# Kernel optimization log

Hardware: AMD Instinct MI355X
Metric: run time of the kernel (lower is better)

## Reference

```python
import jax, jax.numpy as jnp
import numpy as np

B, T, F_IN = 8, 32768, 64
N, F, HID = 64, 64, 32


def setup_inputs() -> dict:
    key = jax.random.key(0)
    ks = jax.random.split(key, 10)
    x = jax.random.normal(ks[0], (B, T, F_IN), dtype=jnp.float32)
    # pre_mlp: Dense(32) -> relu -> Dense(F)
    W1 = jax.random.normal(ks[1], (F_IN, HID), dtype=jnp.float32) * (1.0 / np.sqrt(F_IN))
    b1 = jnp.zeros((HID,), dtype=jnp.float32)
    W2 = jax.random.normal(ks[2], (HID, F), dtype=jnp.float32) * (1.0 / np.sqrt(HID))
    b2 = jnp.zeros((F,), dtype=jnp.float32)
    # SSM params (inits mirror the flax module)
    Lambda_raw = -0.7 * jnp.ones((N,), dtype=jnp.float32)
    P = jax.random.normal(ks[3], (N,), dtype=jnp.float32) * 0.02
    Wu = jax.random.normal(ks[4], (F,), dtype=jnp.float32) * 0.02
    C = jax.random.normal(ks[5], (N,), dtype=jnp.float32) * 0.02
    D = jax.random.normal(ks[6], (F,), dtype=jnp.float32) * 0.02
    b_y = jnp.zeros((), dtype=jnp.float32)
    return {"x": x, "W1": W1, "b1": b1, "W2": W2, "b2": b2,
            "Lambda_raw": Lambda_raw, "P": P, "Wu": Wu, "C": C, "D": D, "b_y": b_y}


def reference(x, W1, b1, W2, b2, Lambda_raw, P, Wu, C, D, b_y):
    # pre_mlp: per-timestep feature projection
    h = jax.nn.relu(jnp.einsum('bti,ih->bth', x, W1) + b1)
    feats = jnp.einsum('bth,hf->btf', h, W2) + b2          # (B,T,F)
    # scalar drive per timestep
    u = jnp.einsum('btf,f->bt', feats, Wu)                 # (B,T)
    # stable diagonal decay in (0,1): Lambda = -softplus(raw), A = exp(Lambda)
    A = jnp.exp(-jax.nn.softplus(Lambda_raw))              # (N,)
    Bu = u[..., None] * P                                  # (B,T,N) per-step injection

    def step(s, bu_t):                                     # s: (B,N), bu_t: (B,N)
        s = A * s + bu_t
        return s, s

    s0 = jnp.zeros((x.shape[0], Lambda_raw.shape[0]), dtype=x.dtype)
    _, states = jax.lax.scan(step, s0, jnp.swapaxes(Bu, 0, 1))  # (T,B,N)
    states = jnp.swapaxes(states, 0, 1)                    # (B,T,N)
    # readout: C-state + D-feedthrough + bias
    y = jnp.einsum('btn,n->bt', states, C) + jnp.einsum('btf,f->bt', feats, D) + b_y
    return y
```

## Files before the change

kernel.cpp:

```cpp
#include <hip/hip_runtime.h>

#define BB   8
#define TT   32768
#define FIN  64
#define HIDN 32
#define NST  64
#define FFD  64
#define WWIN 256
#define TILE 1024


typedef __attribute__((ext_vector_type(8))) short short8;
typedef __attribute__((ext_vector_type(4))) float f32x4;

static __device__ __forceinline__ unsigned short f2bf(float f) {
    unsigned int u = __builtin_bit_cast(unsigned int, f);
    unsigned int lsb = (u >> 16) & 1u;
    u += 0x7fffu + lsb;
    return (unsigned short)(u >> 16);
}

__global__ __launch_bounds__(256) void setup_kernel(
    const float* __restrict__ W1, const float* __restrict__ W2,
    const float* __restrict__ b2, const float* __restrict__ Lraw,
    const float* __restrict__ P, const float* __restrict__ Wu,
    const float* __restrict__ C, const float* __restrict__ Dv,
    const float* __restrict__ b_y, float* __restrict__ ws)
{
    int tid = threadIdx.x;
    if (tid < HIDN) {
        float su = 0.f, sd = 0.f;
        for (int f = 0; f < FFD; ++f) {
            float w2 = W2[tid * FFD + f];
            su += w2 * Wu[f];
            sd += w2 * Dv[f];
        }
        ws[tid]      = su;
        ws[32 + tid] = sd;
    }
    if (tid == 64) {
        float cu = 0.f, cd = 0.f;
        for (int f = 0; f < FFD; ++f) { cu += b2[f] * Wu[f]; cd += b2[f] * Dv[f]; }
        ws[64] = cu;
        ws[65] = cd + b_y[0];
    }
    if (tid < WWIN) {
        float acc = 0.f;
        float jf = (float)tid;
        for (int n = 0; n < NST; ++n) {
            float raw = Lraw[n];
            float sp  = fmaxf(raw, 0.f) + log1pf(expf(-fabsf(raw)));
            acc += C[n] * P[n] * __expf(-sp * jf);
        }
        ws[128 + tid] = acc;
    }
    {
        int f    = tid >> 6;
        int lane = tid & 63;
        int khalf = f & 1, ntile = f >> 1;
        int quad = lane >> 4;
        int nn   = (lane & 15) + ntile * 16;
        unsigned short h8[8];
#pragma unroll
        for (int j = 0; j < 8; ++j) {
            int k = khalf * 32 + quad * 8 + j;
            h8[j] = f2bf(W1[k * HIDN + nn]);
        }
        unsigned int w0 = (unsigned int)h8[0] | ((unsigned int)h8[1] << 16);
        unsigned int w1 = (unsigned int)h8[2] | ((unsigned int)h8[3] << 16);
        unsigned int w2 = (unsigned int)h8[4] | ((unsigned int)h8[5] << 16);
        unsigned int w3 = (unsigned int)h8[6] | ((unsigned int)h8[7] << 16);
        ((uint4*)(ws + 512))[tid] = make_uint4(w0, w1, w2, w3);
    }
}

__global__ __launch_bounds__(256) void mlp_kernel(
    const float* __restrict__ x, const float* __restrict__ b1,
    const float* __restrict__ ws, float* __restrict__ u,
    float* __restrict__ yd)
{
    int lane = threadIdx.x & 63;
    int wid  = threadIdx.x >> 6;
    int tile = blockIdx.x * 4 + wid;
    int t0   = tile * 16;
    int m    = lane & 15;
    int quad = lane >> 4;

    const short8* frp = (const short8*)(ws + 512);
    short8 bk0n0 = frp[0 * 64 + lane];
    short8 bk1n0 = frp[1 * 64 + lane];
    short8 bk0n1 = frp[2 * 64 + lane];
    short8 bk1n1 = frp[3 * 64 + lane];

    const float* xr = x + (size_t)(t0 + m) * FIN + quad * 8;
    float4 xa0 = *(const float4*)(xr);
    float4 xa1 = *(const float4*)(xr + 4);
    float4 xb0 = *(const float4*)(xr + 32);
    float4 xb1 = *(const float4*)(xr + 36);

    short8 a0, a1;
    a0[0] = (short)f2bf(xa0.x); a0[1] = (short)f2bf(xa0.y);
    a0[2] = (short)f2bf(xa0.z); a0[3] = (short)f2bf(xa0.w);
    a0[4] = (short)f2bf(xa1.x); a0[5] = (short)f2bf(xa1.y);
    a0[6] = (short)f2bf(xa1.z); a0[7] = (short)f2bf(xa1.w);
    a1[0] = (short)f2bf(xb0.x); a1[1] = (short)f2bf(xb0.y);
    a1[2] = (short)f2bf(xb0.z); a1[3] = (short)f2bf(xb0.w);
    a1[4] = (short)f2bf(xb1.x); a1[5] = (short)f2bf(xb1.y);
    a1[6] = (short)f2bf(xb1.z); a1[7] = (short)f2bf(xb1.w);

    f32x4 acc0 = {0.f, 0.f, 0.f, 0.f};
    f32x4 acc1 = {0.f, 0.f, 0.f, 0.f};
    acc0 = __builtin_amdgcn_mfma_f32_16x16x32_bf16(a0, bk0n0, acc0, 0, 0, 0);
    acc0 = __builtin_amdgcn_mfma_f32_16x16x32_bf16(a1, bk1n0, acc0, 0, 0, 0);
    acc1 = __builtin_amdgcn_mfma_f32_16x16x32_bf16(a0, bk0n1, acc1, 0, 0, 0);
    acc1 = __builtin_amdgcn_mfma_f32_16x16x32_bf16(a1, bk1n1, acc1, 0, 0, 0);

    float b1n0 = b1[m];
    float b1n1 = b1[16 + m];
    float wu0  = ws[m],      wu1 = ws[16 + m];
    float wd0  = ws[32 + m], wd1 = ws[48 + m];
    float cu   = ws[64],     cd  = ws[65];

    float ut[4], yt[4];
#pragma unroll
    for (int r = 0; r < 4; ++r) {
        float h0 = fmaxf(acc0[r] + b1n0, 0.f);
        float h1 = fmaxf(acc1[r] + b1n1, 0.f);
        ut[r] = h0 * wu0 + h1 * wu1;
        yt[r] = h0 * wd0 + h1 * wd1;
    }
#pragma unroll
    for (int mask = 1; mask <= 8; mask <<= 1) {
#pragma unroll
        for (int r = 0; r < 4; ++r) {
            ut[r] += __shfl_xor(ut[r], mask);
            yt[r] += __shfl_xor(yt[r], mask);
        }
    }
    if (m == 0) {
        int row = t0 + quad * 4;
        *(float4*)&u[row]  = make_float4(ut[0] + cu, ut[1] + cu, ut[2] + cu, ut[3] + cu);
        *(float4*)&yd[row] = make_float4(yt[0] + cd, yt[1] + cd, yt[2] + cd, yt[3] + cd);
    }
}

__global__ __launch_bounds__(256) void conv_kernel(
    const float* __restrict__ u, const float* __restrict__ K,
    float* __restrict__ y)
{
    __shared__ __align__(16) float us[WWIN + TILE];
    __shared__ __align__(16) float Ks[WWIN];

    int tid = threadIdx.x;
    const int blocksPerSeq = TT / TILE;
    int b  = blockIdx.x / blocksPerSeq;
    int t0 = (blockIdx.x % blocksPerSeq) * TILE;
    const float* ub = u + (size_t)b * TT;

    for (int s = tid; s < WWIN + TILE; s += 256) {
        int gt = t0 - WWIN + s;
        us[s] = (gt >= 0) ? ub[gt] : 0.f;
    }
    if (tid < WWIN) Ks[tid] = K[tid];
    __syncthreads();

    int base = WWIN + tid * 4;
    size_t oidx = (size_t)b * TT + t0 + tid * 4;
    float4 yv = *(const float4*)&y[oidx];
    float a0 = yv.x, a1 = yv.y, a2 = yv.z, a3 = yv.w;

#pragma unroll 8
    for (int j = 0; j < WWIN; j += 4) {
        float4 kk = *(const float4*)&Ks[j];
        float4 ua = *(const float4*)&us[base - j - 4];
        float4 ux = *(const float4*)&us[base - j];
        a0 += kk.x * ux.x + kk.y * ua.w + kk.z * ua.z + kk.w * ua.y;
        a1 += kk.x * ux.y + kk.y * ux.x + kk.z * ua.w + kk.w * ua.z;
        a2 += kk.x * ux.z + kk.y * ux.y + kk.z * ux.x + kk.w * ua.w;
        a3 += kk.x * ux.w + kk.y * ux.z + kk.z * ux.y + kk.w * ux.x;
    }
    *(float4*)&y[oidx] = make_float4(a0, a1, a2, a3);
}

extern "C" void kernel_launch(void* const* d_in, const int* in_sizes, int n_in,
                              void* d_out, int out_size, void* d_ws, size_t ws_size,
                              hipStream_t stream)
{
    const float* x    = (const float*)d_in[0];
    const float* W1   = (const float*)d_in[1];
    const float* b1   = (const float*)d_in[2];
    const float* W2   = (const float*)d_in[3];
    const float* b2   = (const float*)d_in[4];
    const float* Lraw = (const float*)d_in[5];
    const float* P    = (const float*)d_in[6];
    const float* Wu   = (const float*)d_in[7];
    const float* C    = (const float*)d_in[8];
    const float* Dv   = (const float*)d_in[9];
    const float* b_y  = (const float*)d_in[10];

    float* ws = (float*)d_ws;
    float* u  = ws + 2048;
    float* y  = (float*)d_out;

    setup_kernel<<<1, 256, 0, stream>>>(W1, W2, b2, Lraw, P, Wu, C, Dv, b_y, ws);
    mlp_kernel<<<(BB * TT / 16) / 4, 256, 0, stream>>>(x, b1, ws, u, y);
    conv_kernel<<<(BB * TT) / TILE, 256, 0, stream>>>(u, ws + 128, y);
}
```

Baseline: 140.7 us.

## Fold setup kernel into MLP and conv kernels, process four tiles per wave

```diff
diff --git a/kernel.cpp b/kernel.cpp
--- a/kernel.cpp
+++ b/kernel.cpp
@@ -8,7 +8,7 @@
 #define FFD  64
 #define WWIN 256
 #define TILE 1024
-
+#define TPW  4
 
 typedef __attribute__((ext_vector_type(8))) short short8;
 typedef __attribute__((ext_vector_type(4))) float f32x4;
@@ -20,136 +20,172 @@
     return (unsigned short)(u >> 16);
 }
 
-__global__ __launch_bounds__(256) void setup_kernel(
-    const float* __restrict__ W1, const float* __restrict__ W2,
-    const float* __restrict__ b2, const float* __restrict__ Lraw,
-    const float* __restrict__ P, const float* __restrict__ Wu,
-    const float* __restrict__ C, const float* __restrict__ Dv,
-    const float* __restrict__ b_y, float* __restrict__ ws)
+static __device__ __forceinline__ float dot8(float4 a0, float4 a1, float4 b0, float4 b1) {
+    return a0.x*b0.x + a0.y*b0.y + a0.z*b0.z + a0.w*b0.w
+         + a1.x*b1.x + a1.y*b1.y + a1.z*b1.z + a1.w*b1.w;
+}
+
+__global__ __launch_bounds__(256) void mlp_kernel(
+    const float* __restrict__ x, const float* __restrict__ W1,
+    const float* __restrict__ b1, const float* __restrict__ W2,
+    const float* __restrict__ b2, const float* __restrict__ Wu,
+    const float* __restrict__ Dv, const float* __restrict__ b_y,
+    float* __restrict__ u, float* __restrict__ yd)
 {
+    __shared__ __align__(16) uint4 fragLDS[4 * 64];
+    __shared__ float pu[32 * 8], pd[32 * 8], pc[16];
+    __shared__ float wuF[32], wdF[32], cucd[2];
+
     int tid = threadIdx.x;
-    if (tid < HIDN) {
-        float su = 0.f, sd = 0.f;
-        for (int f = 0; f < FFD; ++f) {
-            float w2 = W2[tid * FFD + f];
-            su += w2 * Wu[f];
-            sd += w2 * Dv[f];
-        }
-        ws[tid]      = su;
-        ws[32 + tid] = sd;
-    }
-    if (tid == 64) {
-        float cu = 0.f, cd = 0.f;
-        for (int f = 0; f < FFD; ++f) { cu += b2[f] * Wu[f]; cd += b2[f] * Dv[f]; }
-        ws[64] = cu;
-        ws[65] = cd + b_y[0];
-    }
-    if (tid < WWIN) {
-        float acc = 0.f;
-        float jf = (float)tid;
-        for (int n = 0; n < NST; ++n) {
-            float raw = Lraw[n];
-            float sp  = fmaxf(raw, 0.f) + log1pf(expf(-fabsf(raw)));
-            acc += C[n] * P[n] * __expf(-sp * jf);
-        }
-        ws[128 + tid] = acc;
-    }
+
     {
         int f    = tid >> 6;
         int lane = tid & 63;
         int khalf = f & 1, ntile = f >> 1;
-        int quad = lane >> 4;
-        int nn   = (lane & 15) + ntile * 16;
+        int quad  = lane >> 4;
+        int nn    = (lane & 15) + ntile * 16;
         unsigned short h8[8];
 #pragma unroll
         for (int j = 0; j < 8; ++j) {
             int k = khalf * 32 + quad * 8 + j;
             h8[j] = f2bf(W1[k * HIDN + nn]);
         }
-        unsigned int w0 = (unsigned int)h8[0] | ((unsigned int)h8[1] << 16);
-        unsigned int w1 = (unsigned int)h8[2] | ((unsigned int)h8[3] << 16);
-        unsigned int w2 = (unsigned int)h8[4] | ((unsigned int)h8[5] << 16);
-        unsigned int w3 = (unsigned int)h8[6] | ((unsigned int)h8[7] << 16);
-        ((uint4*)(ws + 512))[tid] = make_uint4(w0, w1, w2, w3);
-    }
-}
-
-__global__ __launch_bounds__(256) void mlp_kernel(
-    const float* __restrict__ x, const float* __restrict__ b1,
-    const float* __restrict__ ws, float* __restrict__ u,
-    float* __restrict__ yd)
-{
-    int lane = threadIdx.x & 63;
-    int wid  = threadIdx.x >> 6;
-    int tile = blockIdx.x * 4 + wid;
-    int t0   = tile * 16;
-    int m    = lane & 15;
-    int quad = lane >> 4;
-
-    const short8* frp = (const short8*)(ws + 512);
-    short8 bk0n0 = frp[0 * 64 + lane];
-    short8 bk1n0 = frp[1 * 64 + lane];
-    short8 bk0n1 = frp[2 * 64 + lane];
-    short8 bk1n1 = frp[3 * 64 + lane];
-
-    const float* xr = x + (size_t)(t0 + m) * FIN + quad * 8;
-    float4 xa0 = *(const float4*)(xr);
-    float4 xa1 = *(const float4*)(xr + 4);
-    float4 xb0 = *(const float4*)(xr + 32);
-    float4 xb1 = *(const float4*)(xr + 36);
-
-    short8 a0, a1;
-    a0[0] = (short)f2bf(xa0.x); a0[1] = (short)f2bf(xa0.y);
-    a0[2] = (short)f2bf(xa0.z); a0[3] = (short)f2bf(xa0.w);
-    a0[4] = (short)f2bf(xa1.x); a0[5] = (short)f2bf(xa1.y);
-    a0[6] = (short)f2bf(xa1.z); a0[7] = (short)f2bf(xa1.w);
-    a1[0] = (short)f2bf(xb0.x); a1[1] = (short)f2bf(xb0.y);
-    a1[2] = (short)f2bf(xb0.z); a1[3] = (short)f2bf(xb0.w);
-    a1[4] = (short)f2bf(xb1.x); a1[5] = (short)f2bf(xb1.y);
-    a1[6] = (short)f2bf(xb1.z); a1[7] = (short)f2bf(xb1.w);
-
-    f32x4 acc0 = {0.f, 0.f, 0.f, 0.f};
-    f32x4 acc1 = {0.f, 0.f, 0.f, 0.f};
-    acc0 = __builtin_amdgcn_mfma_f32_16x16x32_bf16(a0, bk0n0, acc0, 0, 0, 0);
-    acc0 = __builtin_amdgcn_mfma_f32_16x16x32_bf16(a1, bk1n0, acc0, 0, 0, 0);
-    acc1 = __builtin_amdgcn_mfma_f32_16x16x32_bf16(a0, bk0n1, acc1, 0, 0, 0);
-    acc1 = __builtin_amdgcn_mfma_f32_16x16x32_bf16(a1, bk1n1, acc1, 0, 0, 0);
-
-    float b1n0 = b1[m];
-    float b1n1 = b1[16 + m];
-    float wu0  = ws[m],      wu1 = ws[16 + m];
-    float wd0  = ws[32 + m], wd1 = ws[48 + m];
-    float cu   = ws[64],     cd  = ws[65];
-
-    float ut[4], yt[4];
-#pragma unroll
-    for (int r = 0; r < 4; ++r) {
-        float h0 = fmaxf(acc0[r] + b1n0, 0.f);
-        float h1 = fmaxf(acc1[r] + b1n1, 0.f);
-        ut[r] = h0 * wu0 + h1 * wu1;
-        yt[r] = h0 * wd0 + h1 * wd1;
-    }
-#pragma unroll
-    for (int mask = 1; mask <= 8; mask <<= 1) {
+        fragLDS[tid] = make_uint4(
+            (unsigned int)h8[0] | ((unsigned int)h8[1] << 16),
+            (unsigned int)h8[2] | ((unsigned int)h8[3] << 16),
+            (unsigned int)h8[4] | ((unsigned int)h8[5] << 16),
+            (unsigned int)h8[6] | ((unsigned int)h8[7] << 16));
+    }
+    {
+        int h = tid >> 3, part = tid & 7;
+        const float4* w2p = (const float4*)(W2 + h * FFD + part * 8);
+        float4 wa = w2p[0], wb = w2p[1];
+        float4 ua = *(const float4*)(Wu + part * 8);
+        float4 ub = *(const float4*)(Wu + part * 8 + 4);
+        float4 da = *(const float4*)(Dv + part * 8);
+        float4 db = *(const float4*)(Dv + part * 8 + 4);
+        pu[tid] = dot8(wa, wb, ua, ub);
+        pd[tid] = dot8(wa, wb, da, db);
+        if (tid < 8) {
+            float4 ba = *(const float4*)(b2 + tid * 8);
+            float4 bb = *(const float4*)(b2 + tid * 8 + 4);
+            float4 u2a = *(const float4*)(Wu + tid * 8);
+            float4 u2b = *(const float4*)(Wu + tid * 8 + 4);
+            pc[tid] = dot8(ba, bb, u2a, u2b);
+        } else if (tid < 16) {
+            int p = tid - 8;
+            float4 ba = *(const float4*)(b2 + p * 8);
+            float4 bb = *(const float4*)(b2 + p * 8 + 4);
+            float4 d2a = *(const float4*)(Dv + p * 8);
+            float4 d2b = *(const float4*)(Dv + p * 8 + 4);
+            pc[tid] = dot8(ba, bb, d2a, d2b);
+        }
+    }
+    __syncthreads();
+    if (tid < 32) {
+        float s = 0.f;
+#pragma unroll
+        for (int p = 0; p < 8; ++p) s += pu[tid * 8 + p];
+        wuF[tid] = s;
+    } else if (tid < 64) {
+        int h = tid - 32;
+        float s = 0.f;
+#pragma unroll
+        for (int p = 0; p < 8; ++p) s += pd[h * 8 + p];
+        wdF[h] = s;
+    } else if (tid == 64) {
+        float s = 0.f;
+#pragma unroll
+        for (int p = 0; p < 8; ++p) s += pc[p];
+        cucd[0] = s;
+    } else if (tid == 65) {
+        float s = 0.f;
+#pragma unroll
+        for (int p = 8; p < 16; ++p) s += pc[p];
+        cucd[1] = s + b_y[0];
+    }
+    __syncthreads();
+
+    int lane = tid & 63, wid = tid >> 6;
+    int m = lane & 15, quad = lane >> 4;
+
+    short8 bk0n0 = __builtin_bit_cast(short8, fragLDS[0 * 64 + lane]);
+    short8 bk1n0 = __builtin_bit_cast(short8, fragLDS[1 * 64 + lane]);
+    short8 bk0n1 = __builtin_bit_cast(short8, fragLDS[2 * 64 + lane]);
+    short8 bk1n1 = __builtin_bit_cast(short8, fragLDS[3 * 64 + lane]);
+
+    float b1n0 = b1[m],       b1n1 = b1[16 + m];
+    float wu0  = wuF[m],      wu1  = wuF[16 + m];
+    float wd0  = wdF[m],      wd1  = wdF[16 + m];
+    float cu   = cucd[0],     cd   = cucd[1];
+
+    int tbase = blockIdx.x * 256 + wid * 64;
+    const float* xr = x + (size_t)(tbase + m) * FIN + quad * 8;
+
+    float4 xv[2][4];
+#define LOADT(buf, tt) { const float* p_ = xr + (tt) * 16 * FIN;          \
+        (buf)[0] = *(const float4*)(p_);      (buf)[1] = *(const float4*)(p_ + 4);  \
+        (buf)[2] = *(const float4*)(p_ + 32); (buf)[3] = *(const float4*)(p_ + 36); }
+
+    LOADT(xv[0], 0);
+    LOADT(xv[1], 1);
+
+#pragma unroll
+    for (int tt = 0; tt < TPW; ++tt) {
+        float4 x0 = xv[tt & 1][0], x1 = xv[tt & 1][1];
+        float4 x2 = xv[tt & 1][2], x3 = xv[tt & 1][3];
+        if (tt + 2 < TPW) LOADT(xv[tt & 1], tt + 2);
+
+        short8 a0, a1;
+        a0[0] = (short)f2bf(x0.x); a0[1] = (short)f2bf(x0.y);
+        a0[2] = (short)f2bf(x0.z); a0[3] = (short)f2bf(x0.w);
+        a0[4] = (short)f2bf(x1.x); a0[5] = (short)f2bf(x1.y);
+        a0[6] = (short)f2bf(x1.z); a0[7] = (short)f2bf(x1.w);
+        a1[0] = (short)f2bf(x2.x); a1[1] = (short)f2bf(x2.y);
+        a1[2] = (short)f2bf(x2.z); a1[3] = (short)f2bf(x2.w);
+        a1[4] = (short)f2bf(x3.x); a1[5] = (short)f2bf(x3.y);
+        a1[6] = (short)f2bf(x3.z); a1[7] = (short)f2bf(x3.w);
+
+        f32x4 acc0 = {0.f, 0.f, 0.f, 0.f};
+        f32x4 acc1 = {0.f, 0.f, 0.f, 0.f};
+        acc0 = __builtin_amdgcn_mfma_f32_16x16x32_bf16(a0, bk0n0, acc0, 0, 0, 0);
+        acc0 = __builtin_amdgcn_mfma_f32_16x16x32_bf16(a1, bk1n0, acc0, 0, 0, 0);
+        acc1 = __builtin_amdgcn_mfma_f32_16x16x32_bf16(a0, bk0n1, acc1, 0, 0, 0);
+        acc1 = __builtin_amdgcn_mfma_f32_16x16x32_bf16(a1, bk1n1, acc1, 0, 0, 0);
+
+        float ut[4], yt[4];
 #pragma unroll
         for (int r = 0; r < 4; ++r) {
-            ut[r] += __shfl_xor(ut[r], mask);
-            yt[r] += __shfl_xor(yt[r], mask);
-        }
-    }
-    if (m == 0) {
-        int row = t0 + quad * 4;
-        *(float4*)&u[row]  = make_float4(ut[0] + cu, ut[1] + cu, ut[2] + cu, ut[3] + cu);
-        *(float4*)&yd[row] = make_float4(yt[0] + cd, yt[1] + cd, yt[2] + cd, yt[3] + cd);
-    }
+            float h0 = fmaxf(acc0[r] + b1n0, 0.f);
+            float h1 = fmaxf(acc1[r] + b1n1, 0.f);
+            ut[r] = h0 * wu0 + h1 * wu1;
+            yt[r] = h0 * wd0 + h1 * wd1;
+        }
+#pragma unroll
+        for (int mask = 1; mask <= 8; mask <<= 1) {
+#pragma unroll
+            for (int r = 0; r < 4; ++r) {
+                ut[r] += __shfl_xor(ut[r], mask);
+                yt[r] += __shfl_xor(yt[r], mask);
+            }
+        }
+        if (m == 0) {
+            int row = tbase + tt * 16 + quad * 4;
+            *(float4*)&u[row]  = make_float4(ut[0] + cu, ut[1] + cu, ut[2] + cu, ut[3] + cu);
+            *(float4*)&yd[row] = make_float4(yt[0] + cd, yt[1] + cd, yt[2] + cd, yt[3] + cd);
+        }
+    }
+#undef LOADT
 }
 
 __global__ __launch_bounds__(256) void conv_kernel(
-    const float* __restrict__ u, const float* __restrict__ K,
+    const float* __restrict__ u, const float* __restrict__ Lraw,
+    const float* __restrict__ P, const float* __restrict__ C,
     float* __restrict__ y)
 {
     __shared__ __align__(16) float us[WWIN + TILE];
     __shared__ __align__(16) float Ks[WWIN];
+    __shared__ float spv[NST], cpv[NST];
 
     int tid = threadIdx.x;
     const int blocksPerSeq = TT / TILE;
@@ -161,7 +197,19 @@
         int gt = t0 - WWIN + s;
         us[s] = (gt >= 0) ? ub[gt] : 0.f;
     }
-    if (tid < WWIN) Ks[tid] = K[tid];
+    if (tid < NST) {
+        float raw = Lraw[tid];
+        spv[tid] = fmaxf(raw, 0.f) + log1pf(expf(-fabsf(raw)));
+        cpv[tid] = C[tid] * P[tid];
+    }
+    __syncthreads();
+    {
+        float jf = (float)tid;
+        float acc = 0.f;
+#pragma unroll 4
+        for (int n = 0; n < NST; ++n) acc += cpv[n] * __expf(-spv[n] * jf);
+        Ks[tid] = acc;
+    }
     __syncthreads();
 
     int base = WWIN + tid * 4;
@@ -198,11 +246,9 @@
     const float* Dv   = (const float*)d_in[9];
     const float* b_y  = (const float*)d_in[10];
 
-    float* ws = (float*)d_ws;
-    float* u  = ws + 2048;
-    float* y  = (float*)d_out;
-
-    setup_kernel<<<1, 256, 0, stream>>>(W1, W2, b2, Lraw, P, Wu, C, Dv, b_y, ws);
-    mlp_kernel<<<(BB * TT / 16) / 4, 256, 0, stream>>>(x, b1, ws, u, y);
-    conv_kernel<<<(BB * TT) / TILE, 256, 0, stream>>>(u, ws + 128, y);
-}
+    float* u = (float*)d_ws;
+    float* y = (float*)d_out;
+
+    mlp_kernel<<<(BB * TT) / 256, 256, 0, stream>>>(x, W1, b1, W2, b2, Wu, Dv, b_y, u, y);
+    conv_kernel<<<(BB * TT) / TILE, 256, 0, stream>>>(u, Lraw, P, C, y);
+}
```

New measurement: 123.4 us. -12.3%, faster.
